# Kernel optimization log

Hardware: AMD Instinct MI355X
Metric: run time of the kernel (lower is better)

The kernel has to match this reference:

```python
import jax, jax.numpy as jnp
import numpy as np

N_EMBD = 1024
N_HEAD = 16
BLOCK_SIZE = 2048
NEG_INF = -1e10


def _rope_cache(head_dim, max_positions):
    # theta_i = 10000^{-2i/dim}, freqs[t, i] = t * theta_i
    theta = 1.0 / (10000.0 ** (jnp.arange(0, head_dim, 2, dtype=jnp.float32) / head_dim))
    freqs = jnp.arange(max_positions, dtype=jnp.float32)[:, None] * theta[None, :]
    return jnp.cos(freqs), jnp.sin(freqs)  # each (max_positions, head_dim//2)


def _apply_rope(x, cos, sin):
    # x: (B, nh, T, hs) interpreted as interleaved complex pairs
    B, nh, T, hs = x.shape
    xr = x.reshape(B, nh, T, hs // 2, 2)
    x0, x1 = xr[..., 0], xr[..., 1]
    c = cos[:T][None, None, :, :]
    s = sin[:T][None, None, :, :]
    o0 = x0 * c - x1 * s
    o1 = x0 * s + x1 * c
    return jnp.stack([o0, o1], axis=-1).reshape(B, nh, T, hs)


def setup_inputs() -> dict:
    key = jax.random.key(0)
    ks = jax.random.split(key, 9)
    B, T, C = 2, 2048, N_EMBD
    sc = 1.0 / np.sqrt(C)
    return {
        "x": jax.random.normal(ks[0], (B, T, C), jnp.float32),
        "Wq": jax.random.normal(ks[1], (C, C), jnp.float32) * sc,
        "bq": jax.random.normal(ks[2], (C,), jnp.float32) * 0.02,
        "Wk": jax.random.normal(ks[3], (C, C), jnp.float32) * sc,
        "bk": jax.random.normal(ks[4], (C,), jnp.float32) * 0.02,
        "Wv": jax.random.normal(ks[5], (C, C), jnp.float32) * sc,
        "bv": jax.random.normal(ks[6], (C,), jnp.float32) * 0.02,
        "Wp": jax.random.normal(ks[7], (C, C), jnp.float32) * sc,
        "bp": jax.random.normal(ks[8], (C,), jnp.float32) * 0.02,
    }


def reference(x, Wq, bq, Wk, bk, Wv, bv, Wp, bp):
    B, T, C = x.shape
    nh, hs = N_HEAD, C // N_HEAD

    def heads(W, b):
        return (x @ W.T + b).reshape(B, T, nh, hs).transpose(0, 2, 1, 3)

    q = heads(Wq, bq)
    k = heads(Wk, bk)
    v = heads(Wv, bv)

    cos, sin = _rope_cache(hs, BLOCK_SIZE)
    q = _apply_rope(q, cos, sin)
    k = _apply_rope(k, cos, sin)

    att = jnp.einsum("bhqd,bhkd->bhqk", q, k) * (1.0 / np.sqrt(hs))
    causal = jnp.tril(jnp.ones((T, T), dtype=bool))
    att = jnp.where(causal[None, None], att, NEG_INF)
    att = jax.nn.softmax(att, axis=-1)
    y = jnp.einsum("bhqk,bhkd->bhqd", att, v)
    y = y.transpose(0, 2, 1, 3).reshape(B, T, C)
    return y @ Wp.T + bp
```

## Files before the change

kernel.cpp:

```cpp
#include <hip/hip_runtime.h>

typedef __bf16 bf16;
typedef short  s16;
typedef s16   s16x8 __attribute__((ext_vector_type(8)));
typedef bf16  bf16x4 __attribute__((ext_vector_type(4)));
typedef float f32x4 __attribute__((ext_vector_type(4)));

#define B_SZ 2
#define T_SEQ 2048
#define C_DIM 1024
#define NH 16
#define HS 64
#define M_TOT (B_SZ * T_SEQ)

#define NEG_BIG (-30000.0f)
#define LOG2_10000 13.287712379549449f

__device__ __forceinline__ float san(float x) {
    unsigned u = __float_as_uint(x);
    return ((u & 0x7F800000u) == 0x7F800000u) ? 0.f : x;
}

__device__ __forceinline__ void load16_lds(const bf16* g, void* lds_base) {
    __builtin_amdgcn_global_load_lds(
        (const __attribute__((address_space(1))) void*)g,
        (__attribute__((address_space(3))) void*)lds_base, 16, 0, 0);
}

template <int N>
__device__ __forceinline__ float row_ror(float x) {
    return __int_as_float(__builtin_amdgcn_mov_dpp(
        __float_as_int(x), 0x120 + N, 0xf, 0xf, true));
}
__device__ __forceinline__ float rowmax16(float x) {
    x = fmaxf(x, row_ror<1>(x));
    x = fmaxf(x, row_ror<2>(x));
    x = fmaxf(x, row_ror<4>(x));
    x = fmaxf(x, row_ror<8>(x));
    return x;
}
__device__ __forceinline__ float rowsum16(float x) {
    x += row_ror<1>(x);
    x += row_ror<2>(x);
    x += row_ror<4>(x);
    x += row_ror<8>(x);
    return x;
}

__global__ __launch_bounds__(256) void cvt_bf16_kernel(
    const float* __restrict__ x,  const float* __restrict__ wq,
    const float* __restrict__ wk, const float* __restrict__ wv,
    const float* __restrict__ wp,
    bf16* __restrict__ xb, bf16* __restrict__ wqb, bf16* __restrict__ wkb,
    bf16* __restrict__ wvb, bf16* __restrict__ wpb)
{
    const int z = blockIdx.y;
    const float* src = (z == 0) ? x : (z == 1) ? wq : (z == 2) ? wk : (z == 3) ? wv : wp;
    bf16* dst = (z == 0) ? xb : (z == 1) ? wqb : (z == 2) ? wkb : (z == 3) ? wvb : wpb;
    const int n = (z == 0) ? (M_TOT * C_DIM) : (C_DIM * C_DIM);

    const int i = (blockIdx.x * 256 + threadIdx.x) * 4;
    if (i >= n) return;
    const float4 v = *(const float4*)(src + i);
    bf16x4 o;
    o[0] = (bf16)v.x; o[1] = (bf16)v.y; o[2] = (bf16)v.z; o[3] = (bf16)v.w;
    *(bf16x4*)(dst + i) = o;
}

__global__ __launch_bounds__(256) void rope_tab_kernel(float* __restrict__ cs,
                                                       float* __restrict__ sn)
{
    const int idx = blockIdx.x * 256 + threadIdx.x;
    const int t = idx >> 5, i = idx & 31;
    const float theta = __builtin_exp2f(-(float)(2 * i) * (LOG2_10000 / 64.f));
    const float a = (float)t * theta;
    cs[idx] = san(cosf(a));
    sn[idx] = san(sinf(a));
}

#define GEMM_CORE(Xp, Wp_)                                                     \
    const int t = threadIdx.x;                                                 \
    const int w = t >> 6;                                                      \
    const int lane = t & 63;                                                   \
    const int qd = lane >> 4;                                                  \
    const int r  = lane & 15;                                                  \
    const int wm = w & 1, wn = w >> 1;                                         \
    const int srow = t >> 2;                                                   \
    const int scol = (t & 3) * 8;                                              \
    const bf16* gA0 = (Xp) + (size_t)(m0 + srow) * C_DIM + scol;               \
    const bf16* gA1 = (Xp) + (size_t)(m0 + 64 + srow) * C_DIM + scol;          \
    const bf16* gB0 = (Wp_) + (size_t)(n0 + srow) * C_DIM + scol;              \
    const bf16* gB1 = (Wp_) + (size_t)(n0 + 64 + srow) * C_DIM + scol;         \
    char* ldsA0 = (char*)sA + (size_t)(w * 64) * 16;                           \
    char* ldsA1 = (char*)sA + (size_t)(256 + w * 64) * 16;                     \
    char* ldsB0 = (char*)sB + (size_t)(w * 64) * 16;                           \
    char* ldsB1 = (char*)sB + (size_t)(256 + w * 64) * 16;                     \
    f32x4 acc[4][4] = {};                                                      \
    for (int k0 = 0; k0 < C_DIM; k0 += 32) {                                   \
        __syncthreads();                                                       \
        load16_lds(gA0 + k0, ldsA0);                                           \
        load16_lds(gA1 + k0, ldsA1);                                           \
        load16_lds(gB0 + k0, ldsB0);                                           \
        load16_lds(gB1 + k0, ldsB1);                                           \
        __syncthreads();                                                       \
        s16x8 af[4], bfr[4];                                                   \
        _Pragma("unroll")                                                      \
        for (int mt = 0; mt < 4; mt++)                                         \
            af[mt] = *(const s16x8*)(sA + (wm * 64 + mt * 16 + r) * 32 + qd * 8); \
        _Pragma("unroll")                                                      \
        for (int nt = 0; nt < 4; nt++)                                         \
            bfr[nt] = *(const s16x8*)(sB + (wn * 64 + nt * 16 + r) * 32 + qd * 8); \
        _Pragma("unroll")                                                      \
        for (int mt = 0; mt < 4; mt++)                                         \
            _Pragma("unroll")                                                  \
            for (int nt = 0; nt < 4; nt++)                                     \
                acc[mt][nt] = __builtin_amdgcn_mfma_f32_16x16x32_bf16(         \
                    af[mt], bfr[nt], acc[mt][nt], 0, 0, 0);                    \
    }

__global__ __launch_bounds__(256) void qkv_gemm(
    const bf16* __restrict__ X,
    const bf16* __restrict__ Wq, const float* __restrict__ bq,
    const bf16* __restrict__ Wk, const float* __restrict__ bk,
    const bf16* __restrict__ Wv, const float* __restrict__ bv,
    const float* __restrict__ cs_tab, const float* __restrict__ sn_tab,
    bf16* __restrict__ q_ws, bf16* __restrict__ k_ws, bf16* __restrict__ vt_ws)
{
    __shared__ __attribute__((aligned(16))) bf16 sA[128 * 32];
    __shared__ __attribute__((aligned(16))) bf16 sB[128 * 32];

    const int mode = blockIdx.z;
    const bf16*  Wm   = (mode == 0) ? Wq : (mode == 1) ? Wk : Wv;
    const float* bias = (mode == 0) ? bq : (mode == 1) ? bk : bv;
    const int m0 = blockIdx.x * 128;
    const int n0 = blockIdx.y * 128;

    GEMM_CORE(X, Wm)

    if (mode == 2) {
        #pragma unroll
        for (int mt = 0; mt < 4; mt++) {
            const int mrow0 = m0 + wm * 64 + mt * 16 + qd * 4;
            const int bb = mrow0 >> 11;
            const int t0 = mrow0 & 2047;
            #pragma unroll
            for (int nt = 0; nt < 4; nt++) {
                const int col = n0 + wn * 64 + nt * 16 + r;
                const int h = col >> 6, d = col & 63;
                const float bv_ = bias[col];
                bf16x4 pk;
                #pragma unroll
                for (int reg = 0; reg < 4; reg++)
                    pk[reg] = (bf16)san(acc[mt][nt][reg] + bv_);
                *(bf16x4*)(vt_ws + ((size_t)(bb * NH + h) * HS + d) * T_SEQ + t0) = pk;
            }
        }
    } else {
        bf16* out = (mode == 0) ? q_ws : k_ws;
        #pragma unroll
        for (int mt = 0; mt < 4; mt++) {
            const int mrow0 = m0 + wm * 64 + mt * 16 + qd * 4;
            const int bb = mrow0 >> 11;
            const int t0 = mrow0 & 2047;
            #pragma unroll
            for (int nt = 0; nt < 4; nt++) {
                const int col = n0 + wn * 64 + nt * 16 + r;
                const int h = col >> 6, d = col & 63;
                const int pi = d >> 1;
                const float bv_ = bias[col];
                #pragma unroll
                for (int reg = 0; reg < 4; reg++) {
                    const int tt = t0 + reg;
                    float v = san(acc[mt][nt][reg] + bv_);
                    float partner = __shfl_xor(v, 1);
                    float c = cs_tab[tt * 32 + pi];
                    float s = sn_tab[tt * 32 + pi];
                    float rot = (d & 1) ? (v * c + partner * s)
                                        : (v * c - partner * s);
                    out[((size_t)(bb * NH + h) * T_SEQ + tt) * HS + d] = (bf16)san(rot);
                }
            }
        }
    }
}

__global__ __launch_bounds__(256) void proj_gemm(
    const bf16* __restrict__ Y, const bf16* __restrict__ Wp,
    const float* __restrict__ bp, float* __restrict__ out)
{
    __shared__ __attribute__((aligned(16))) bf16 sA[128 * 32];
    __shared__ __attribute__((aligned(16))) bf16 sB[128 * 32];

    const int m0 = blockIdx.x * 128;
    const int n0 = blockIdx.y * 128;

    GEMM_CORE(Y, Wp)

    #pragma unroll
    for (int mt = 0; mt < 4; mt++) {
        const int mrow0 = m0 + wm * 64 + mt * 16 + qd * 4;
        #pragma unroll
        for (int nt = 0; nt < 4; nt++) {
            const int col = n0 + wn * 64 + nt * 16 + r;
            const float bv_ = bp[col];
            #pragma unroll
            for (int reg = 0; reg < 4; reg++)
                out[(size_t)(mrow0 + reg) * C_DIM + col] = san(acc[mt][nt][reg] + bv_);
        }
    }
}

__global__ __launch_bounds__(256) void attn_kernel(
    const bf16* __restrict__ q_ws, const bf16* __restrict__ k_ws,
    const bf16* __restrict__ vt_ws, bf16* __restrict__ y_ws)
{
    __shared__ __attribute__((aligned(16))) bf16 sK[2][2][64][32];
    __shared__ __attribute__((aligned(16))) bf16 sV[2][2][64][32];
    __shared__ __attribute__((aligned(16))) bf16 sP[4][16][72];

    const int bx = blockIdx.x;
    const int bh = blockIdx.y;
    const int w    = threadIdx.x >> 6;
    const int lane = threadIdx.x & 63;
    const int qd = lane >> 4;
    const int r  = lane & 15;

    const bf16* Qb = q_ws + (size_t)bh * T_SEQ * HS;
    const bf16* Kb = k_ws + (size_t)bh * T_SEQ * HS;
    const bf16* Vb = vt_ws + (size_t)bh * HS * T_SEQ;

    const int srow = lane >> 2;
    const int scol = (lane & 3) * 8;
    const bf16* Kb_w = Kb + (size_t)(w * 16 + srow) * HS + scol;
    const bf16* Vb_w = Vb + (size_t)(w * 16 + srow) * T_SEQ + scol;

    bf16 (*pw)[72] = sP[w];
    const int bb = bh >> 4, h = bh & 15;

    #pragma unroll 1
    for (int phase = 0; phase < 2; phase++) {
        const int qt = phase ? bx : (T_SEQ / 64 - 1 - bx);
        const int q0 = qt * 64 + w * 16;

        s16x8 aq0 = *(const s16x8*)(Qb + (size_t)(q0 + r) * HS + qd * 8);
        s16x8 aq1 = *(const s16x8*)(Qb + (size_t)(q0 + r) * HS + 32 + qd * 8);

        f32x4 o[4] = {};
        float m_i[4], l_i[4];
        #pragma unroll
        for (int j = 0; j < 4; j++) { m_i[j] = NEG_BIG; l_i[j] = 0.f; }

        __syncthreads();
        load16_lds(Kb_w,      &sK[0][0][w * 16][0]);
        load16_lds(Kb_w + 32, &sK[0][1][w * 16][0]);
        load16_lds(Vb_w,      &sV[0][0][w * 16][0]);
        load16_lds(Vb_w + 32, &sV[0][1][w * 16][0]);

        for (int kt = 0; kt <= qt; kt++) {
            const int cur = kt & 1;
            __syncthreads();

            if (kt < qt) {
                const bf16* kp = Kb_w + (size_t)(kt + 1) * 64 * HS;
                const bf16* vp = Vb_w + (kt + 1) * 64;
                load16_lds(kp,      &sK[cur ^ 1][0][w * 16][0]);
                load16_lds(kp + 32, &sK[cur ^ 1][1][w * 16][0]);
                load16_lds(vp,      &sV[cur ^ 1][0][w * 16][0]);
                load16_lds(vp + 32, &sV[cur ^ 1][1][w * 16][0]);
            }

            f32x4 s[4];
            #pragma unroll
            for (int nt = 0; nt < 4; nt++) {
                s16x8 b0 = *(const s16x8*)&sK[cur][0][nt * 16 + r][qd * 8];
                s16x8 b1 = *(const s16x8*)&sK[cur][1][nt * 16 + r][qd * 8];
                f32x4 z = {};
                z = __builtin_amdgcn_mfma_f32_16x16x32_bf16(aq0, b0, z, 0, 0, 0);
                z = __builtin_amdgcn_mfma_f32_16x16x32_bf16(aq1, b1, z, 0, 0, 0);
                s[nt] = z;
            }

            const float scale = 0.125f;
            if (kt == qt) {
                #pragma unroll
                for (int nt = 0; nt < 4; nt++)
                    #pragma unroll
                    for (int reg = 0; reg < 4; reg++) {
                        const int qg = q0 + qd * 4 + reg;
                        const int kg = kt * 64 + nt * 16 + r;
                        s[nt][reg] = (kg <= qg) ? s[nt][reg] * scale : NEG_BIG;
                    }
            } else {
                #pragma unroll
                for (int nt = 0; nt < 4; nt++)
                    #pragma unroll
                    for (int reg = 0; reg < 4; reg++) s[nt][reg] *= scale;
            }

            float mnew[4], alpha[4];
            #pragma unroll
            for (int reg = 0; reg < 4; reg++) {
                float mx = fmaxf(fmaxf(s[0][reg], s[1][reg]),
                                 fmaxf(s[2][reg], s[3][reg]));
                mx = rowmax16(mx);
                mnew[reg] = fmaxf(m_i[reg], mx);
                alpha[reg] = __expf(fminf(m_i[reg] - mnew[reg], 0.f));
                m_i[reg] = mnew[reg];
            }
            float rs[4];
            #pragma unroll
            for (int reg = 0; reg < 4; reg++) rs[reg] = 0.f;
            #pragma unroll
            for (int nt = 0; nt < 4; nt++)
                #pragma unroll
                for (int reg = 0; reg < 4; reg++) {
                    float p = __expf(fminf(s[nt][reg] - mnew[reg], 0.f));
                    s[nt][reg] = p;
                    rs[reg] += p;
                }
            #pragma unroll
            for (int reg = 0; reg < 4; reg++)
                l_i[reg] = l_i[reg] * alpha[reg] + rowsum16(rs[reg]);
            #pragma unroll
            for (int nt = 0; nt < 4; nt++)
                #pragma unroll
                for (int reg = 0; reg < 4; reg++) o[nt][reg] *= alpha[reg];

            #pragma unroll
            for (int nt = 0; nt < 4; nt++)
                #pragma unroll
                for (int reg = 0; reg < 4; reg++)
                    pw[qd * 4 + reg][nt * 16 + r] = (bf16)s[nt][reg];

            s16x8 ap0 = *(const s16x8*)&pw[r][qd * 8];
            s16x8 ap1 = *(const s16x8*)&pw[r][32 + qd * 8];
            #pragma unroll
            for (int nt = 0; nt < 4; nt++) {
                s16x8 bv0 = *(const s16x8*)&sV[cur][0][nt * 16 + r][qd * 8];
                s16x8 bv1 = *(const s16x8*)&sV[cur][1][nt * 16 + r][qd * 8];
                o[nt] = __builtin_amdgcn_mfma_f32_16x16x32_bf16(ap0, bv0, o[nt], 0, 0, 0);
                o[nt] = __builtin_amdgcn_mfma_f32_16x16x32_bf16(ap1, bv1, o[nt], 0, 0, 0);
            }
        }

        #pragma unroll
        for (int reg = 0; reg < 4; reg++) {
            const int tq = q0 + qd * 4 + reg;
            const float inv = 1.f / fmaxf(l_i[reg], 1e-20f);
            bf16* dst = y_ws + ((size_t)(bb * T_SEQ + tq) * NH + h) * HS;
            #pragma unroll
            for (int nt = 0; nt < 4; nt++)
                dst[nt * 16 + r] = (bf16)san(o[nt][reg] * inv);
        }
    }
}

extern "C" void kernel_launch(void* const* d_in, const int* in_sizes, int n_in,
                              void* d_out, int out_size, void* d_ws, size_t ws_size,
                              hipStream_t stream)
{
    const size_t MB = 1024 * 1024;
    const size_t NEED = 40 * MB + 2 * 65536 * sizeof(float);
    if (ws_size < NEED || n_in < 9) return;

    const float* x  = (const float*)d_in[0];
    const float* Wq = (const float*)d_in[1];
    const float* bq = (const float*)d_in[2];
    const float* Wk = (const float*)d_in[3];
    const float* bk = (const float*)d_in[4];
    const float* Wv = (const float*)d_in[5];
    const float* bv = (const float*)d_in[6];
    const float* Wp = (const float*)d_in[7];
    const float* bp = (const float*)d_in[8];
    float* out = (float*)d_out;

    char* ws = (char*)d_ws;
    bf16*  q_ws   = (bf16*)(ws + 0 * MB);
    bf16*  k_ws   = (bf16*)(ws + 8 * MB);
    bf16*  vt_ws  = (bf16*)(ws + 16 * MB);
    bf16*  x_b    = (bf16*)(ws + 24 * MB);
    bf16*  y_ws   = (bf16*)(ws + 24 * MB);
    bf16*  Wq_b   = (bf16*)(ws + 32 * MB);
    bf16*  Wk_b   = (bf16*)(ws + 34 * MB);
    bf16*  Wv_b   = (bf16*)(ws + 36 * MB);
    bf16*  Wp_b   = (bf16*)(ws + 38 * MB);
    float* cs_tab = (float*)(ws + 40 * MB);
    float* sn_tab = cs_tab + 65536;

    cvt_bf16_kernel<<<dim3(M_TOT * C_DIM / 4 / 256, 5), 256, 0, stream>>>(
        x, Wq, Wk, Wv, Wp, x_b, Wq_b, Wk_b, Wv_b, Wp_b);
    rope_tab_kernel<<<dim3(65536 / 256), 256, 0, stream>>>(cs_tab, sn_tab);
    qkv_gemm<<<dim3(M_TOT / 128, C_DIM / 128, 3), 256, 0, stream>>>(
        x_b, Wq_b, bq, Wk_b, bk, Wv_b, bv, cs_tab, sn_tab, q_ws, k_ws, vt_ws);
    attn_kernel<<<dim3(T_SEQ / 128, B_SZ * NH), 256, 0, stream>>>(
        q_ws, k_ws, vt_ws, y_ws);
    proj_gemm<<<dim3(M_TOT / 128, C_DIM / 128), 256, 0, stream>>>(
        y_ws, Wp_b, bp, out);
}
```

Measured before the change: 223.6 us.

## Split causal attention KV range across two blocks and fold softmax scale into Q

Attention now runs as a split-KV pass: each 64-row query tile's causal key range is halved between two blocks. Each block writes unnormalized partial outputs plus row max and sum, and a new combine kernel merges them into the final output. This launches four times as many attention blocks, aiming to fill the GPU better and balance the uneven causal work. Separately, Q is pre-multiplied by 1/sqrt(hs)*log2(e) in the QKV epilogue, so softmax uses exp2 with no per-score scale multiply. The cost is an extra kernel launch and extra global traffic for the bf16 partials, and the split path only runs if the workspace is at least 59 MB.

Measured after the change: 263.1 us. 17.7% more time.

```diff
diff --git a/kernel.cpp b/kernel.cpp
--- a/kernel.cpp
+++ b/kernel.cpp
@@ -15,6 +15,7 @@
 
 #define NEG_BIG (-30000.0f)
 #define LOG2_10000 13.287712379549449f
+#define Q_PRESCALE 0.18033688011112042f
 
 __device__ __forceinline__ float san(float x) {
     unsigned u = __float_as_uint(x);
@@ -157,6 +158,7 @@
         }
     } else {
         bf16* out = (mode == 0) ? q_ws : k_ws;
+        const float post = (mode == 0) ? Q_PRESCALE : 1.0f;
         #pragma unroll
         for (int mt = 0; mt < 4; mt++) {
             const int mrow0 = m0 + wm * 64 + mt * 16 + qd * 4;
@@ -177,7 +179,8 @@
                     float s = sn_tab[tt * 32 + pi];
                     float rot = (d & 1) ? (v * c + partner * s)
                                         : (v * c - partner * s);
-                    out[((size_t)(bb * NH + h) * T_SEQ + tt) * HS + d] = (bf16)san(rot);
+                    out[((size_t)(bb * NH + h) * T_SEQ + tt) * HS + d] =
+                        (bf16)san(rot * post);
                 }
             }
         }
@@ -210,6 +213,178 @@
     }
 }
 
+#define ATTN_TILE_BODY(cur, is_diag)                                           \
+    {                                                                          \
+        f32x4 s[4];                                                            \
+        _Pragma("unroll")                                                      \
+        for (int nt = 0; nt < 4; nt++) {                                       \
+            s16x8 b0 = *(const s16x8*)&sK[cur][0][nt * 16 + r][qd * 8];        \
+            s16x8 b1 = *(const s16x8*)&sK[cur][1][nt * 16 + r][qd * 8];        \
+            f32x4 z = {};                                                      \
+            z = __builtin_amdgcn_mfma_f32_16x16x32_bf16(aq0, b0, z, 0, 0, 0);  \
+            z = __builtin_amdgcn_mfma_f32_16x16x32_bf16(aq1, b1, z, 0, 0, 0);  \
+            s[nt] = z;                                                         \
+        }                                                                      \
+        if (is_diag) {                                                         \
+            _Pragma("unroll")                                                  \
+            for (int nt = 0; nt < 4; nt++)                                     \
+                _Pragma("unroll")                                              \
+                for (int reg = 0; reg < 4; reg++) {                            \
+                    const int qg = q0 + qd * 4 + reg;                          \
+                    const int kg = kt * 64 + nt * 16 + r;                      \
+                    s[nt][reg] = (kg <= qg) ? s[nt][reg] : NEG_BIG;            \
+                }                                                              \
+        }                                                                      \
+        float mnew[4], alpha[4];                                               \
+        _Pragma("unroll")                                                      \
+        for (int reg = 0; reg < 4; reg++) {                                    \
+            float mx = fmaxf(fmaxf(s[0][reg], s[1][reg]),                      \
+                             fmaxf(s[2][reg], s[3][reg]));                     \
+            mx = rowmax16(mx);                                                 \
+            mnew[reg] = fmaxf(m_i[reg], mx);                                   \
+            alpha[reg] = __builtin_exp2f(fminf(m_i[reg] - mnew[reg], 0.f));    \
+            m_i[reg] = mnew[reg];                                              \
+        }                                                                      \
+        float rs[4];                                                           \
+        _Pragma("unroll")                                                      \
+        for (int reg = 0; reg < 4; reg++) rs[reg] = 0.f;                       \
+        _Pragma("unroll")                                                      \
+        for (int nt = 0; nt < 4; nt++)                                         \
+            _Pragma("unroll")                                                  \
+            for (int reg = 0; reg < 4; reg++) {                                \
+                float p = __builtin_exp2f(fminf(s[nt][reg] - mnew[reg], 0.f)); \
+                s[nt][reg] = p;                                                \
+                rs[reg] += p;                                                  \
+            }                                                                  \
+        _Pragma("unroll")                                                      \
+        for (int reg = 0; reg < 4; reg++)                                      \
+            l_i[reg] = l_i[reg] * alpha[reg] + rowsum16(rs[reg]);              \
+        _Pragma("unroll")                                                      \
+        for (int nt = 0; nt < 4; nt++)                                         \
+            _Pragma("unroll")                                                  \
+            for (int reg = 0; reg < 4; reg++) o[nt][reg] *= alpha[reg];        \
+        _Pragma("unroll")                                                      \
+        for (int nt = 0; nt < 4; nt++)                                         \
+            _Pragma("unroll")                                                  \
+            for (int reg = 0; reg < 4; reg++)                                  \
+                pw[qd * 4 + reg][nt * 16 + r] = (bf16)s[nt][reg];              \
+        s16x8 ap0 = *(const s16x8*)&pw[r][qd * 8];                             \
+        s16x8 ap1 = *(const s16x8*)&pw[r][32 + qd * 8];                        \
+        _Pragma("unroll")                                                      \
+        for (int nt = 0; nt < 4; nt++) {                                       \
+            s16x8 bv0 = *(const s16x8*)&sV[cur][0][nt * 16 + r][qd * 8];       \
+            s16x8 bv1 = *(const s16x8*)&sV[cur][1][nt * 16 + r][qd * 8];       \
+            o[nt] = __builtin_amdgcn_mfma_f32_16x16x32_bf16(ap0, bv0, o[nt], 0, 0, 0); \
+            o[nt] = __builtin_amdgcn_mfma_f32_16x16x32_bf16(ap1, bv1, o[nt], 0, 0, 0); \
+        }                                                                      \
+    }
+
+__global__ __launch_bounds__(256) void attn_part(
+    const bf16* __restrict__ q_ws, const bf16* __restrict__ k_ws,
+    const bf16* __restrict__ vt_ws,
+    bf16* __restrict__ o_p, float2* __restrict__ ml_p)
+{
+    __shared__ __attribute__((aligned(16))) bf16 sK[2][2][64][32];
+    __shared__ __attribute__((aligned(16))) bf16 sV[2][2][64][32];
+    __shared__ __attribute__((aligned(16))) bf16 sP[4][16][72];
+
+    const int bx = blockIdx.x;
+    const int qt = (T_SEQ / 64 - 1) - (bx >> 1);
+    const int half = bx & 1;
+    const int bh = blockIdx.y;
+    const int mid = (qt + 2) >> 1;
+    const int lo = half ? mid : 0;
+    const int hi = half ? (qt + 1) : mid;
+
+    const int w    = threadIdx.x >> 6;
+    const int lane = threadIdx.x & 63;
+    const int qd = lane >> 4;
+    const int r  = lane & 15;
+
+    const bf16* Qb = q_ws + (size_t)bh * T_SEQ * HS;
+    const bf16* Kb = k_ws + (size_t)bh * T_SEQ * HS;
+    const bf16* Vb = vt_ws + (size_t)bh * HS * T_SEQ;
+
+    const int q0 = qt * 64 + w * 16;
+    s16x8 aq0 = *(const s16x8*)(Qb + (size_t)(q0 + r) * HS + qd * 8);
+    s16x8 aq1 = *(const s16x8*)(Qb + (size_t)(q0 + r) * HS + 32 + qd * 8);
+
+    const int srow = lane >> 2;
+    const int scol = (lane & 3) * 8;
+    const bf16* Kb_w = Kb + (size_t)(w * 16 + srow) * HS + scol;
+    const bf16* Vb_w = Vb + (size_t)(w * 16 + srow) * T_SEQ + scol;
+
+    f32x4 o[4] = {};
+    float m_i[4], l_i[4];
+    #pragma unroll
+    for (int j = 0; j < 4; j++) { m_i[j] = NEG_BIG; l_i[j] = 0.f; }
+    bf16 (*pw)[72] = sP[w];
+
+    if (lo < hi) {
+        const bf16* kp = Kb_w + (size_t)lo * 64 * HS;
+        const bf16* vp = Vb_w + lo * 64;
+        load16_lds(kp,      &sK[lo & 1][0][w * 16][0]);
+        load16_lds(kp + 32, &sK[lo & 1][1][w * 16][0]);
+        load16_lds(vp,      &sV[lo & 1][0][w * 16][0]);
+        load16_lds(vp + 32, &sV[lo & 1][1][w * 16][0]);
+    }
+
+    for (int kt = lo; kt < hi; kt++) {
+        const int cur = kt & 1;
+        __syncthreads();
+        if (kt + 1 < hi) {
+            const bf16* kp = Kb_w + (size_t)(kt + 1) * 64 * HS;
+            const bf16* vp = Vb_w + (kt + 1) * 64;
+            load16_lds(kp,      &sK[cur ^ 1][0][w * 16][0]);
+            load16_lds(kp + 32, &sK[cur ^ 1][1][w * 16][0]);
+            load16_lds(vp,      &sV[cur ^ 1][0][w * 16][0]);
+            load16_lds(vp + 32, &sV[cur ^ 1][1][w * 16][0]);
+        }
+        ATTN_TILE_BODY(cur, (kt == qt))
+    }
+
+    const size_t base = ((size_t)(qt * 2 + half) * (B_SZ * NH) + bh) * 64;
+    #pragma unroll
+    for (int reg = 0; reg < 4; reg++) {
+        const int row = w * 16 + qd * 4 + reg;
+        bf16* dst = o_p + (base + row) * 64;
+        #pragma unroll
+        for (int nt = 0; nt < 4; nt++)
+            dst[nt * 16 + r] = (bf16)san(o[nt][reg]);
+        if (r == 0) ml_p[base + row] = make_float2(m_i[reg], l_i[reg]);
+    }
+}
+
+__global__ __launch_bounds__(256) void attn_combine(
+    const bf16* __restrict__ o_p, const float2* __restrict__ ml_p,
+    bf16* __restrict__ y_ws)
+{
+    const int qt = blockIdx.x;
+    const int bh = blockIdx.y;
+    const int tid = threadIdx.x;
+    const int row = tid >> 2;
+    const int d0  = (tid & 3) * 16;
+
+    const size_t b1 = ((size_t)(qt * 2 + 0) * (B_SZ * NH) + bh) * 64 + row;
+    const size_t b2 = ((size_t)(qt * 2 + 1) * (B_SZ * NH) + bh) * 64 + row;
+    const float2 ml1 = ml_p[b1];
+    const float2 ml2 = ml_p[b2];
+    const float m = fmaxf(ml1.x, ml2.x);
+    const float a1 = __builtin_exp2f(fminf(ml1.x - m, 0.f));
+    const float a2 = __builtin_exp2f(fminf(ml2.x - m, 0.f));
+    const float inv = 1.f / fmaxf(ml1.y * a1 + ml2.y * a2, 1e-20f);
+    const float c1 = a1 * inv, c2 = a2 * inv;
+
+    const int bb = bh >> 4, h = bh & 15;
+    const int trow = qt * 64 + row;
+    bf16* dst = y_ws + ((size_t)(bb * T_SEQ + trow) * NH + h) * HS + d0;
+    const bf16* p1 = o_p + b1 * 64 + d0;
+    const bf16* p2 = o_p + b2 * 64 + d0;
+    #pragma unroll
+    for (int j = 0; j < 16; j++)
+        dst[j] = (bf16)san((float)p1[j] * c1 + (float)p2[j] * c2);
+}
+
 __global__ __launch_bounds__(256) void attn_kernel(
     const bf16* __restrict__ q_ws, const bf16* __restrict__ k_ws,
     const bf16* __restrict__ vt_ws, bf16* __restrict__ y_ws)
@@ -259,7 +434,6 @@
         for (int kt = 0; kt <= qt; kt++) {
             const int cur = kt & 1;
             __syncthreads();
-
             if (kt < qt) {
                 const bf16* kp = Kb_w + (size_t)(kt + 1) * 64 * HS;
                 const bf16* vp = Vb_w + (kt + 1) * 64;
@@ -268,79 +442,7 @@
                 load16_lds(vp,      &sV[cur ^ 1][0][w * 16][0]);
                 load16_lds(vp + 32, &sV[cur ^ 1][1][w * 16][0]);
             }
-
-            f32x4 s[4];
-            #pragma unroll
-            for (int nt = 0; nt < 4; nt++) {
-                s16x8 b0 = *(const s16x8*)&sK[cur][0][nt * 16 + r][qd * 8];
-                s16x8 b1 = *(const s16x8*)&sK[cur][1][nt * 16 + r][qd * 8];
-                f32x4 z = {};
-                z = __builtin_amdgcn_mfma_f32_16x16x32_bf16(aq0, b0, z, 0, 0, 0);
-                z = __builtin_amdgcn_mfma_f32_16x16x32_bf16(aq1, b1, z, 0, 0, 0);
-                s[nt] = z;
-            }
-
-            const float scale = 0.125f;
-            if (kt == qt) {
-                #pragma unroll
-                for (int nt = 0; nt < 4; nt++)
-                    #pragma unroll
-                    for (int reg = 0; reg < 4; reg++) {
-                        const int qg = q0 + qd * 4 + reg;
-                        const int kg = kt * 64 + nt * 16 + r;
-                        s[nt][reg] = (kg <= qg) ? s[nt][reg] * scale : NEG_BIG;
-                    }
-            } else {
-                #pragma unroll
-                for (int nt = 0; nt < 4; nt++)
-                    #pragma unroll
-                    for (int reg = 0; reg < 4; reg++) s[nt][reg] *= scale;
-            }
-
-            float mnew[4], alpha[4];
-            #pragma unroll
-            for (int reg = 0; reg < 4; reg++) {
-                float mx = fmaxf(fmaxf(s[0][reg], s[1][reg]),
-                                 fmaxf(s[2][reg], s[3][reg]));
-                mx = rowmax16(mx);
-                mnew[reg] = fmaxf(m_i[reg], mx);
-                alpha[reg] = __expf(fminf(m_i[reg] - mnew[reg], 0.f));
-                m_i[reg] = mnew[reg];
-            }
-            float rs[4];
-            #pragma unroll
-            for (int reg = 0; reg < 4; reg++) rs[reg] = 0.f;
-            #pragma unroll
-            for (int nt = 0; nt < 4; nt++)
-                #pragma unroll
-                for (int reg = 0; reg < 4; reg++) {
-                    float p = __expf(fminf(s[nt][reg] - mnew[reg], 0.f));
-                    s[nt][reg] = p;
-                    rs[reg] += p;
-                }
-            #pragma unroll
-            for (int reg = 0; reg < 4; reg++)
-                l_i[reg] = l_i[reg] * alpha[reg] + rowsum16(rs[reg]);
-            #pragma unroll
-            for (int nt = 0; nt < 4; nt++)
-                #pragma unroll
-                for (int reg = 0; reg < 4; reg++) o[nt][reg] *= alpha[reg];
-
-            #pragma unroll
-            for (int nt = 0; nt < 4; nt++)
-                #pragma unroll
-                for (int reg = 0; reg < 4; reg++)
-                    pw[qd * 4 + reg][nt * 16 + r] = (bf16)s[nt][reg];
-
-            s16x8 ap0 = *(const s16x8*)&pw[r][qd * 8];
-            s16x8 ap1 = *(const s16x8*)&pw[r][32 + qd * 8];
-            #pragma unroll
-            for (int nt = 0; nt < 4; nt++) {
-                s16x8 bv0 = *(const s16x8*)&sV[cur][0][nt * 16 + r][qd * 8];
-                s16x8 bv1 = *(const s16x8*)&sV[cur][1][nt * 16 + r][qd * 8];
-                o[nt] = __builtin_amdgcn_mfma_f32_16x16x32_bf16(ap0, bv0, o[nt], 0, 0, 0);
-                o[nt] = __builtin_amdgcn_mfma_f32_16x16x32_bf16(ap1, bv1, o[nt], 0, 0, 0);
-            }
+            ATTN_TILE_BODY(cur, (kt == qt))
         }
 
         #pragma unroll
@@ -360,8 +462,9 @@
                               hipStream_t stream)
 {
     const size_t MB = 1024 * 1024;
-    const size_t NEED = 40 * MB + 2 * 65536 * sizeof(float);
-    if (ws_size < NEED || n_in < 9) return;
+    const size_t NEED_BASE  = 40 * MB + 2 * 65536 * sizeof(float);
+    const size_t NEED_SPLIT = 59 * MB;
+    if (ws_size < NEED_BASE || n_in < 9) return;
 
     const float* x  = (const float*)d_in[0];
     const float* Wq = (const float*)d_in[1];
@@ -386,14 +489,25 @@
     bf16*  Wp_b   = (bf16*)(ws + 38 * MB);
     float* cs_tab = (float*)(ws + 40 * MB);
     float* sn_tab = cs_tab + 65536;
+    bf16*   o_p   = (bf16*)(ws + 41 * MB);
+    float2* ml_p  = (float2*)(ws + 58 * MB);
 
     cvt_bf16_kernel<<<dim3(M_TOT * C_DIM / 4 / 256, 5), 256, 0, stream>>>(
         x, Wq, Wk, Wv, Wp, x_b, Wq_b, Wk_b, Wv_b, Wp_b);
     rope_tab_kernel<<<dim3(65536 / 256), 256, 0, stream>>>(cs_tab, sn_tab);
     qkv_gemm<<<dim3(M_TOT / 128, C_DIM / 128, 3), 256, 0, stream>>>(
         x_b, Wq_b, bq, Wk_b, bk, Wv_b, bv, cs_tab, sn_tab, q_ws, k_ws, vt_ws);
-    attn_kernel<<<dim3(T_SEQ / 128, B_SZ * NH), 256, 0, stream>>>(
-        q_ws, k_ws, vt_ws, y_ws);
+
+    if (ws_size >= NEED_SPLIT) {
+        attn_part<<<dim3(T_SEQ / 64 * 2, B_SZ * NH), 256, 0, stream>>>(
+            q_ws, k_ws, vt_ws, o_p, ml_p);
+        attn_combine<<<dim3(T_SEQ / 64, B_SZ * NH), 256, 0, stream>>>(
+            o_p, ml_p, y_ws);
+    } else {
+        attn_kernel<<<dim3(T_SEQ / 128, B_SZ * NH), 256, 0, stream>>>(
+            q_ws, k_ws, vt_ws, y_ws);
+    }
+
     proj_gemm<<<dim3(M_TOT / 128, C_DIM / 128), 256, 0, stream>>>(
         y_ws, Wp_b, bp, out);
 }
```
